# Kernel tuning notes

Measured on AMD Instinct MI355X. Metric: run time of the kernel, lower is better.

Reference implementation:

```python
import jax, jax.numpy as jnp
import numpy as np

DIM = 256
NUM_HEADS = 4
HEAD_DIM = DIM // NUM_HEADS  # 64
SCALE = HEAD_DIM ** -0.5


def _dwconv(x, w, b):
    # x: [B,H,W,C], w: [3,3,1,C] depthwise, stride 2, padding 1
    c = x.shape[-1]
    y = jax.lax.conv_general_dilated(
        x, w, window_strides=(2, 2), padding=((1, 1), (1, 1)),
        dimension_numbers=('NHWC', 'HWIO', 'NHWC'), feature_group_count=c)
    return y + b


def setup_inputs() -> dict:
    key = jax.random.key(0)
    ks = jax.random.split(key, 12)
    s = 0.02
    return {
        'x': jax.random.normal(ks[0], (8, 64, 64, DIM), jnp.float32),
        'q_w': jax.random.normal(ks[1], (DIM, DIM), jnp.float32) * s,
        'q_b': jnp.zeros((DIM,), jnp.float32),
        'k_w': jax.random.normal(ks[2], (DIM, HEAD_DIM), jnp.float32) * s,
        'k_b': jnp.zeros((HEAD_DIM,), jnp.float32),
        'v_w': jax.random.normal(ks[3], (DIM, HEAD_DIM), jnp.float32) * s,
        'v_b': jnp.zeros((HEAD_DIM,), jnp.float32),
        'kconv_w': jax.random.normal(ks[4], (3, 3, 1, HEAD_DIM), jnp.float32) * s,
        'kconv_b': jnp.zeros((HEAD_DIM,), jnp.float32),
        'vconv_w': jax.random.normal(ks[5], (3, 3, 1, HEAD_DIM), jnp.float32) * s,
        'vconv_b': jnp.zeros((HEAD_DIM,), jnp.float32),
        'out_w': jax.random.normal(ks[6], (DIM, DIM), jnp.float32) * s,
        'out_b': jnp.zeros((DIM,), jnp.float32),
    }


def reference(x, q_w, q_b, k_w, k_b, v_w, v_b,
              kconv_w, kconv_b, vconv_w, vconv_b, out_w, out_b):
    B, H, W, _ = x.shape
    S = H * W
    q = x @ q_w + q_b                      # [B,H,W,DIM]
    k = x @ k_w + k_b                      # [B,H,W,HEAD_DIM]
    v = x @ v_w + v_b
    k = _dwconv(k, kconv_w, kconv_b)       # [B,H/2,W/2,HEAD_DIM]
    v = _dwconv(v, vconv_w, vconv_b)
    Kv = (H // 2) * (W // 2)
    q = q.reshape(B, S, NUM_HEADS, HEAD_DIM)
    k = k.reshape(B, Kv, HEAD_DIM)
    v = v.reshape(B, Kv, HEAD_DIM)
    # MQA: single shared K/V head
    attn = jnp.einsum('bqhd,bkd->bhqk', q, k) * SCALE
    attn = jax.nn.softmax(attn, axis=-1)
    out = jnp.einsum('bhqk,bkd->bqhd', attn, v)   # [B,S,nh,hd]
    out = out.reshape(B, S, DIM) @ out_w + out_b
    return out.reshape(B, H, W, DIM)
```

## Files before the change

### kernel.cpp

```cpp
#include <hip/hip_runtime.h>
#include <hip/hip_bf16.h>

typedef __bf16 v8bf __attribute__((ext_vector_type(8)));
typedef float f32x4 __attribute__((ext_vector_type(4)));
typedef float f32x16 __attribute__((ext_vector_type(16)));
typedef int v2i __attribute__((ext_vector_type(2)));
typedef int v4i __attribute__((ext_vector_type(4)));

#define MFMA16(a, b, c) __builtin_amdgcn_mfma_f32_16x16x32_bf16(a, b, c, 0, 0, 0)
#define MFMA32(a, b, c) __builtin_amdgcn_mfma_f32_32x32x16_bf16(a, b, c, 0, 0, 0)
#define GLOAD16(gp, lp)                                                        \
  __builtin_amdgcn_global_load_lds(                                            \
      (const __attribute__((address_space(1))) void*)(gp),                     \
      (__attribute__((address_space(3))) void*)(lp), 16, 0, 0)

#define QSCALE 0.18033688011112042f

__global__ __launch_bounds__(256) void k_cvt_w(const float* __restrict__ qw,
                                               const float* __restrict__ kw,
                                               const float* __restrict__ vw,
                                               const float* __restrict__ ow,
                                               __bf16* __restrict__ wfrag,
                                               __bf16* __restrict__ owfrag) {
  int t = blockIdx.x * 256 + threadIdx.x;
  if (t < 98304) {
    int e = t & 7, idx = t >> 3;
    int l = idx & 63; idx >>= 6;
    int n = idx & 3; idx >>= 2;
    int kk = idx & 7, nb = idx >> 3;
    int nn = nb * 64 + n * 16 + (l & 15);
    int k = kk * 32 + 8 * (l >> 4) + e;
    float v;
    if (nn < 256) v = qw[k * 256 + nn] * QSCALE;
    else if (nn < 320) v = kw[k * 64 + (nn - 256)];
    else v = vw[k * 64 + (nn - 320)];
    wfrag[t] = (__bf16)v;
  } else {
    int u = t - 98304;
    int e = u & 7, idx = u >> 3;
    int l = idx & 63; idx >>= 6;
    int n = idx & 3; idx >>= 2;
    int kk = idx & 7, nb = idx >> 3;
    int nn = nb * 64 + n * 16 + (l & 15);
    int k = kk * 32 + 8 * (l >> 4) + e;
    owfrag[u] = (__bf16)ow[k * 256 + nn];
  }
}

__global__ __launch_bounds__(256) void k_qkv(const float* __restrict__ x,
                                             const __bf16* __restrict__ wfrag,
                                             const float* __restrict__ qb,
                                             const float* __restrict__ kb,
                                             const float* __restrict__ vb,
                                             __bf16* __restrict__ qo,
                                             __bf16* __restrict__ klin,
                                             __bf16* __restrict__ vlin) {
  int bx = blockIdx.x;
  int mb = (bx & 7) * 128 + (bx >> 3);
  int wave = threadIdx.x >> 6, lane = threadIdx.x & 63;
  int rg = wave >> 1, nh = wave & 1;
  int g = lane >> 4, c = lane & 15;
  int r0 = mb * 32 + rg * 16;
  const v8bf* wf = (const v8bf*)wfrag;

  v8bf a[8];
#pragma unroll
  for (int kk = 0; kk < 8; ++kk) {
    const float* ap = x + (size_t)(r0 + c) * 256 + kk * 32 + 8 * g;
    float4 f0 = *(const float4*)ap;
    float4 f1 = *(const float4*)(ap + 4);
    v8bf t;
    t[0] = (__bf16)f0.x; t[1] = (__bf16)f0.y; t[2] = (__bf16)f0.z; t[3] = (__bf16)f0.w;
    t[4] = (__bf16)f1.x; t[5] = (__bf16)f1.y; t[6] = (__bf16)f1.z; t[7] = (__bf16)f1.w;
    a[kk] = t;
  }
#pragma unroll
  for (int ni = 0; ni < 3; ++ni) {
    int nb = nh * 3 + ni;
    int n0 = nb * 64;
    f32x4 acc[4];
#pragma unroll
    for (int n = 0; n < 4; ++n) acc[n] = f32x4{0.f, 0.f, 0.f, 0.f};
#pragma unroll
    for (int kk = 0; kk < 8; ++kk) {
      v8bf bf[4];
#pragma unroll
      for (int n = 0; n < 4; ++n)
        bf[n] = wf[(((nb * 8 + kk) * 4 + n) << 6) | lane];
#pragma unroll
      for (int n = 0; n < 4; ++n) acc[n] = MFMA16(a[kk], bf[n], acc[n]);
    }
#pragma unroll
    for (int n = 0; n < 4; ++n) {
      int col = n0 + n * 16 + c;
      float bias;
      if (col < 256) bias = qb[col] * QSCALE;
      else if (col < 320) bias = kb[col - 256];
      else bias = vb[col - 320];
#pragma unroll
      for (int j = 0; j < 4; ++j) {
        int row = r0 + 4 * g + j;
        float v = acc[n][j] + bias;
        if (col < 256) qo[(size_t)row * 256 + col] = (__bf16)v;
        else if (col < 320) klin[(size_t)row * 64 + (col - 256)] = (__bf16)v;
        else vlin[(size_t)row * 64 + (col - 320)] = (__bf16)v;
      }
    }
  }
}

__global__ __launch_bounds__(256) void k_conv(const __bf16* __restrict__ klin,
                                              const __bf16* __restrict__ vlin,
                                              const float* __restrict__ kw,
                                              const float* __restrict__ kbias,
                                              const float* __restrict__ vw,
                                              const float* __restrict__ vbias,
                                              __bf16* __restrict__ kcS,
                                              __bf16* __restrict__ vcS) {
  int bx = blockIdx.x;
  int phase = bx >> 8;
  int b = (bx >> 5) & 7, tile = bx & 31;
  int u = threadIdx.x;

  if (phase == 0) {
    const __bf16* kin = klin + (size_t)b * 262144;
    int kj = u >> 5, kr = (u & 31) ^ kj;
    float acc[8];
#pragma unroll
    for (int e = 0; e < 8; ++e) acc[e] = kbias[kj * 8 + e];
#pragma unroll
    for (int dy = 0; dy < 3; ++dy) {
      int iy = 2 * tile - 1 + dy;
      if (iy < 0 || iy > 63) continue;
#pragma unroll
      for (int dx = 0; dx < 3; ++dx) {
        int ix = 2 * kr - 1 + dx;
        if (ix < 0 || ix > 63) continue;
        v8bf kv8 = *(const v8bf*)(kin + ((size_t)iy * 64 + ix) * 64 + kj * 8);
        const float* wp = kw + (dy * 3 + dx) * 64 + kj * 8;
#pragma unroll
        for (int e = 0; e < 8; ++e) acc[e] += (float)kv8[e] * wp[e];
      }
    }
    __bf16 o[8];
#pragma unroll
    for (int e = 0; e < 8; ++e) o[e] = (__bf16)acc[e];
    *(v4i*)(kcS + ((size_t)b * 32 + tile) * 2048 + u * 8) = *(v4i*)o;
  } else {
    const __bf16* vin = vlin + (size_t)b * 262144;
    int dt = u >> 7, ks = (u >> 6) & 1, vh = (u >> 5) & 1;
    int cc = (u & 31) ^ (ks * 2 + vh);
    int ch = dt * 32 + cc;
    float vwv[9];
#pragma unroll
    for (int i = 0; i < 9; ++i) vwv[i] = vw[i * 64 + ch];
    float vb0 = vbias[ch];
    __bf16 o[8];
#pragma unroll
    for (int e = 0; e < 8; ++e) {
      int ox = ks * 16 + vh * 8 + e;
      float av = vb0;
#pragma unroll
      for (int dy = 0; dy < 3; ++dy) {
        int iy = 2 * tile - 1 + dy;
        if (iy < 0 || iy > 63) continue;
#pragma unroll
        for (int dx = 0; dx < 3; ++dx) {
          int ix = 2 * ox - 1 + dx;
          if (ix < 0 || ix > 63) continue;
          av += (float)vin[((size_t)iy * 64 + ix) * 64 + ch] * vwv[dy * 3 + dx];
        }
      }
      o[e] = (__bf16)av;
    }
    *(v4i*)(vcS + ((size_t)b * 32 + tile) * 2048 + u * 8) = *(v4i*)o;
  }
}

__global__ __launch_bounds__(256) void k_attn(const __bf16* __restrict__ q,
                                              const __bf16* __restrict__ kcS,
                                              const __bf16* __restrict__ vcS,
                                              const __bf16* __restrict__ owfrag,
                                              const float* __restrict__ ob,
                                              float* __restrict__ out) {
  __shared__ __bf16 SMEM[12288];
  int bx = blockIdx.x;
  int L = (bx & 7) * 128 + (bx >> 3);
  int b = L >> 7, qt = L & 127;
  int wave = threadIdx.x >> 6, lane = threadIdx.x & 63;
  int c = lane & 31, hi = lane >> 5;
  int t = threadIdx.x;
  size_t rowBase = (size_t)b * 4096 + qt * 32;

  const __bf16* kg = kcS + (size_t)b * 65536 + t * 8;
  const __bf16* vg = vcS + (size_t)b * 65536 + t * 8;
  __bf16* kl = &SMEM[t * 8];
  __bf16* vl = &SMEM[2048 + t * 8];

  int Koff[4], Voff[2][2];
#pragma unroll
  for (int kk = 0; kk < 4; ++kk) {
    int j = kk * 2 + hi;
    Koff[kk] = (j * 32 + (c ^ j)) * 8;
  }
#pragma unroll
  for (int ks = 0; ks < 2; ++ks)
#pragma unroll
    for (int dt = 0; dt < 2; ++dt) {
      int j = ks * 2 + hi;
      Voff[ks][dt] = (256 + dt * 128 + ks * 64 + hi * 32 + (c ^ j)) * 8;
    }

  const __bf16* qbase = q + (rowBase + c) * 256 + wave * 64 + hi * 8;
  v8bf Qf[4];
#pragma unroll
  for (int kk = 0; kk < 4; ++kk) Qf[kk] = *(const v8bf*)(qbase + kk * 16);

  f32x16 O0 = {}, O1 = {};
  const f32x16 Z16 = {};
  float ls0 = 0.f, ls1 = 0.f, ls2 = 0.f, ls3 = 0.f;

  GLOAD16(kg, kl);
  GLOAD16(vg, vl);
  GLOAD16(kg + 2048, kl + 4096);
  GLOAD16(vg + 2048, vl + 4096);

  int cur = 0;
  int nxt2 = 2;
  for (int it = 0; it < 32; ++it) {
    if (it < 31) {
      asm volatile("s_waitcnt vmcnt(2)" ::: "memory");
    } else {
      asm volatile("s_waitcnt vmcnt(0)" ::: "memory");
    }
    __builtin_amdgcn_sched_barrier(0);
    __builtin_amdgcn_s_barrier();
    __builtin_amdgcn_sched_barrier(0);
    if (it < 30) {
      GLOAD16(kg + (it + 2) * 2048, kl + nxt2 * 4096);
      GLOAD16(vg + (it + 2) * 2048, vl + nxt2 * 4096);
    }

    const __bf16* base = &SMEM[cur * 4096];
    v8bf Kf[4], Vf[2][2];
#pragma unroll
    for (int kk = 0; kk < 4; ++kk) Kf[kk] = *(const v8bf*)(base + Koff[kk]);
#pragma unroll
    for (int ks = 0; ks < 2; ++ks)
#pragma unroll
      for (int dt = 0; dt < 2; ++dt)
        Vf[ks][dt] = *(const v8bf*)(base + Voff[ks][dt]);

    f32x16 S = MFMA32(Kf[0], Qf[0], Z16);
    S = MFMA32(Kf[1], Qf[1], S);
    S = MFMA32(Kf[2], Qf[2], S);
    S = MFMA32(Kf[3], Qf[3], S);

#pragma unroll
    for (int r = 0; r < 16; ++r) S[r] = __builtin_amdgcn_exp2f(S[r]);
    ls0 += (S[0] + S[1]) + (S[2] + S[3]);
    ls1 += (S[4] + S[5]) + (S[6] + S[7]);
    ls2 += (S[8] + S[9]) + (S[10] + S[11]);
    ls3 += (S[12] + S[13]) + (S[14] + S[15]);

    int w[8];
#pragma unroll
    for (int q2 = 0; q2 < 8; ++q2) {
      int r;
      asm("v_cvt_pk_bf16_f32 %0, %1, %2"
          : "=v"(r) : "v"(S[2 * q2]), "v"(S[2 * q2 + 1]));
      w[q2] = r;
    }
    v2i s1 = __builtin_amdgcn_permlane32_swap(w[2], w[0], false, false);
    v2i s2 = __builtin_amdgcn_permlane32_swap(w[3], w[1], false, false);
    v2i s3 = __builtin_amdgcn_permlane32_swap(w[6], w[4], false, false);
    v2i s4 = __builtin_amdgcn_permlane32_swap(w[7], w[5], false, false);
    v4i pa0i, pa1i;
    pa0i[0] = s1[1]; pa0i[1] = s2[1]; pa0i[2] = s1[0]; pa0i[3] = s2[0];
    pa1i[0] = s3[1]; pa1i[1] = s4[1]; pa1i[2] = s3[0]; pa1i[3] = s4[0];
    v8bf pa0 = *(v8bf*)&pa0i, pa1 = *(v8bf*)&pa1i;

    O0 = MFMA32(pa0, Vf[0][0], O0);
    O1 = MFMA32(pa0, Vf[0][1], O1);
    O0 = MFMA32(pa1, Vf[1][0], O0);
    O1 = MFMA32(pa1, Vf[1][1], O1);

    cur = (cur == 2) ? 0 : cur + 1;
    nxt2 = (nxt2 == 2) ? 0 : nxt2 + 1;
  }

  float lsum = (ls0 + ls1) + (ls2 + ls3);
  float tot = lsum + __shfl_xor(lsum, 32);
  float linv = 1.0f / tot;

  __syncthreads();

  __bf16(*Ot)[264] = (__bf16(*)[264])SMEM;
#pragma unroll
  for (int r = 0; r < 16; ++r) {
    int qr = (r & 3) + 8 * (r >> 2) + 4 * hi;
    float li = __shfl(linv, qr);
    Ot[qr][wave * 64 + c] = (__bf16)(O0[r] * li);
    Ot[qr][wave * 64 + 32 + c] = (__bf16)(O1[r] * li);
  }
  __syncthreads();

  int g = lane >> 4, c16 = lane & 15;
  const v8bf* wf = (const v8bf*)owfrag;
  f32x4 acc[2][4];
#pragma unroll
  for (int m = 0; m < 2; ++m)
#pragma unroll
    for (int n = 0; n < 4; ++n) acc[m][n] = f32x4{0.f, 0.f, 0.f, 0.f};
#pragma unroll
  for (int kk = 0; kk < 8; ++kk) {
    v8bf a0 = *(const v8bf*)&Ot[c16][kk * 32 + 8 * g];
    v8bf a1 = *(const v8bf*)&Ot[16 + c16][kk * 32 + 8 * g];
    v8bf bf[4];
#pragma unroll
    for (int n = 0; n < 4; ++n)
      bf[n] = wf[(((wave * 8 + kk) * 4 + n) << 6) | lane];
#pragma unroll
    for (int n = 0; n < 4; ++n) {
      acc[0][n] = MFMA16(a0, bf[n], acc[0][n]);
      acc[1][n] = MFMA16(a1, bf[n], acc[1][n]);
    }
  }
#pragma unroll
  for (int n = 0; n < 4; ++n) {
    int col = wave * 64 + n * 16 + c16;
    float bias = ob[col];
#pragma unroll
    for (int m = 0; m < 2; ++m)
#pragma unroll
      for (int j = 0; j < 4; ++j) {
        int row = m * 16 + 4 * g + j;
        out[(rowBase + row) * 256 + col] = acc[m][n][j] + bias;
      }
  }
}

extern "C" void kernel_launch(void* const* d_in, const int* in_sizes, int n_in,
                              void* d_out, int out_size, void* d_ws, size_t ws_size,
                              hipStream_t stream) {
  const float* x   = (const float*)d_in[0];
  const float* qw  = (const float*)d_in[1];
  const float* qb  = (const float*)d_in[2];
  const float* kw  = (const float*)d_in[3];
  const float* kb  = (const float*)d_in[4];
  const float* vw  = (const float*)d_in[5];
  const float* vb  = (const float*)d_in[6];
  const float* kcw = (const float*)d_in[7];
  const float* kcb = (const float*)d_in[8];
  const float* vcw = (const float*)d_in[9];
  const float* vcb = (const float*)d_in[10];
  const float* ow  = (const float*)d_in[11];
  const float* ob  = (const float*)d_in[12];
  float* out = (float*)d_out;
  char* ws = (char*)d_ws;

  __bf16* kcS    = (__bf16*)(ws + 0);
  __bf16* vcS    = (__bf16*)(ws + 1048576);
  __bf16* qbuf   = (__bf16*)(ws + 16777216);
  __bf16* klin   = (__bf16*)(ws + 33554432);
  __bf16* vlin   = (__bf16*)(ws + 37748736);
  __bf16* wfrag  = (__bf16*)(ws + 44040192);
  __bf16* owfrag = (__bf16*)(ws + 44236800);

  k_cvt_w<<<640, 256, 0, stream>>>(qw, kw, vw, ow, wfrag, owfrag);
  k_qkv<<<1024, 256, 0, stream>>>(x, wfrag, qb, kb, vb, qbuf, klin, vlin);
  k_conv<<<512, 256, 0, stream>>>(klin, vlin, kcw, kcb, vcw, vcb, kcS, vcS);
  k_attn<<<1024, 256, 0, stream>>>(qbuf, kcS, vcS, owfrag, ob, out);
}
```

Baseline: 89.85 us.

## Double attention block to 64 query rows sharing each K/V tile load

Each attention block now uses 512 threads covering 64 query rows: two row groups of four head-waves. The K/V tiles staged into shared memory are reused by twice as many waves, which halves global K/V traffic per query and halves the block count. Each thread now issues a single async load per stage instead of two, and the out-projection buffer grows to hold 64 rows. The launch bound of 512 threads with 4 blocks per CU may constrain registers, and the larger blocks mean fewer blocks in total across the grid.

```diff
diff --git a/kernel.cpp b/kernel.cpp
--- a/kernel.cpp
+++ b/kernel.cpp
@@ -177,25 +177,26 @@
   }
 }
 
-__global__ __launch_bounds__(256) void k_attn(const __bf16* __restrict__ q,
-                                              const __bf16* __restrict__ kcS,
-                                              const __bf16* __restrict__ vcS,
-                                              const __bf16* __restrict__ owfrag,
-                                              const float* __restrict__ ob,
-                                              float* __restrict__ out) {
-  __shared__ __bf16 SMEM[12288];
+__global__ __launch_bounds__(512, 4) void k_attn(const __bf16* __restrict__ q,
+                                                 const __bf16* __restrict__ kcS,
+                                                 const __bf16* __restrict__ vcS,
+                                                 const __bf16* __restrict__ owfrag,
+                                                 const float* __restrict__ ob,
+                                                 float* __restrict__ out) {
+  __shared__ __bf16 SMEM[16896];
   int bx = blockIdx.x;
-  int L = (bx & 7) * 128 + (bx >> 3);
-  int b = L >> 7, qt = L & 127;
-  int wave = threadIdx.x >> 6, lane = threadIdx.x & 63;
+  int L = (bx & 7) * 64 + (bx >> 3);
+  int b = L >> 6, qt = L & 63;
+  int tid = threadIdx.x;
+  int wave = tid >> 6, lane = tid & 63;
+  int h = wave & 3, rg = wave >> 2;
   int c = lane & 31, hi = lane >> 5;
-  int t = threadIdx.x;
-  size_t rowBase = (size_t)b * 4096 + qt * 32;
-
-  const __bf16* kg = kcS + (size_t)b * 65536 + t * 8;
-  const __bf16* vg = vcS + (size_t)b * 65536 + t * 8;
-  __bf16* kl = &SMEM[t * 8];
-  __bf16* vl = &SMEM[2048 + t * 8];
+  size_t rowBase = (size_t)b * 4096 + qt * 64;
+
+  const __bf16* gsrc = (tid < 256)
+                           ? kcS + (size_t)b * 65536 + tid * 8
+                           : vcS + (size_t)b * 65536 + (tid - 256) * 8;
+  __bf16* ldst = (tid < 256) ? &SMEM[tid * 8] : &SMEM[2048 + (tid - 256) * 8];
 
   int Koff[4], Voff[2][2];
 #pragma unroll
@@ -211,7 +212,7 @@
       Voff[ks][dt] = (256 + dt * 128 + ks * 64 + hi * 32 + (c ^ j)) * 8;
     }
 
-  const __bf16* qbase = q + (rowBase + c) * 256 + wave * 64 + hi * 8;
+  const __bf16* qbase = q + (rowBase + rg * 32 + c) * 256 + h * 64 + hi * 8;
   v8bf Qf[4];
 #pragma unroll
   for (int kk = 0; kk < 4; ++kk) Qf[kk] = *(const v8bf*)(qbase + kk * 16);
@@ -220,16 +221,14 @@
   const f32x16 Z16 = {};
   float ls0 = 0.f, ls1 = 0.f, ls2 = 0.f, ls3 = 0.f;
 
-  GLOAD16(kg, kl);
-  GLOAD16(vg, vl);
-  GLOAD16(kg + 2048, kl + 4096);
-  GLOAD16(vg + 2048, vl + 4096);
+  GLOAD16(gsrc, ldst);
+  GLOAD16(gsrc + 2048, ldst + 4096);
 
   int cur = 0;
   int nxt2 = 2;
   for (int it = 0; it < 32; ++it) {
     if (it < 31) {
-      asm volatile("s_waitcnt vmcnt(2)" ::: "memory");
+      asm volatile("s_waitcnt vmcnt(1)" ::: "memory");
     } else {
       asm volatile("s_waitcnt vmcnt(0)" ::: "memory");
     }
@@ -237,8 +236,7 @@
     __builtin_amdgcn_s_barrier();
     __builtin_amdgcn_sched_barrier(0);
     if (it < 30) {
-      GLOAD16(kg + (it + 2) * 2048, kl + nxt2 * 4096);
-      GLOAD16(vg + (it + 2) * 2048, vl + nxt2 * 4096);
+      GLOAD16(gsrc + (it + 2) * 2048, ldst + nxt2 * 4096);
     }
 
     const __bf16* base = &SMEM[cur * 4096];
@@ -300,8 +298,8 @@
   for (int r = 0; r < 16; ++r) {
     int qr = (r & 3) + 8 * (r >> 2) + 4 * hi;
     float li = __shfl(linv, qr);
-    Ot[qr][wave * 64 + c] = (__bf16)(O0[r] * li);
-    Ot[qr][wave * 64 + 32 + c] = (__bf16)(O1[r] * li);
+    Ot[rg * 32 + qr][h * 64 + c] = (__bf16)(O0[r] * li);
+    Ot[rg * 32 + qr][h * 64 + 32 + c] = (__bf16)(O1[r] * li);
   }
   __syncthreads();
 
@@ -314,12 +312,12 @@
     for (int n = 0; n < 4; ++n) acc[m][n] = f32x4{0.f, 0.f, 0.f, 0.f};
 #pragma unroll
   for (int kk = 0; kk < 8; ++kk) {
-    v8bf a0 = *(const v8bf*)&Ot[c16][kk * 32 + 8 * g];
-    v8bf a1 = *(const v8bf*)&Ot[16 + c16][kk * 32 + 8 * g];
+    v8bf a0 = *(const v8bf*)&Ot[rg * 32 + c16][kk * 32 + 8 * g];
+    v8bf a1 = *(const v8bf*)&Ot[rg * 32 + 16 + c16][kk * 32 + 8 * g];
     v8bf bf[4];
 #pragma unroll
     for (int n = 0; n < 4; ++n)
-      bf[n] = wf[(((wave * 8 + kk) * 4 + n) << 6) | lane];
+      bf[n] = wf[(((h * 8 + kk) * 4 + n) << 6) | lane];
 #pragma unroll
     for (int n = 0; n < 4; ++n) {
       acc[0][n] = MFMA16(a0, bf[n], acc[0][n]);
@@ -328,13 +326,13 @@
   }
 #pragma unroll
   for (int n = 0; n < 4; ++n) {
-    int col = wave * 64 + n * 16 + c16;
+    int col = h * 64 + n * 16 + c16;
     float bias = ob[col];
 #pragma unroll
     for (int m = 0; m < 2; ++m)
 #pragma unroll
       for (int j = 0; j < 4; ++j) {
-        int row = m * 16 + 4 * g + j;
+        int row = rg * 32 + m * 16 + 4 * g + j;
         out[(rowBase + row) * 256 + col] = acc[m][n][j] + bias;
       }
   }
@@ -370,5 +368,5 @@
   k_cvt_w<<<640, 256, 0, stream>>>(qw, kw, vw, ow, wfrag, owfrag);
   k_qkv<<<1024, 256, 0, stream>>>(x, wfrag, qb, kb, vb, qbuf, klin, vlin);
   k_conv<<<512, 256, 0, stream>>>(klin, vlin, kcw, kcb, vcw, vcb, kcS, vcS);
-  k_attn<<<1024, 256, 0, stream>>>(qbuf, kcS, vcS, owfrag, ob, out);
-}
+  k_attn<<<512, 512, 0, stream>>>(qbuf, kcS, vcS, owfrag, ob, out);
+}
```

After: 86.32 us, median of 3. 3.9% less time.

## Load K/V fragments directly from global into registers, drop LDS staging

Applied to the files above, without the earlier changes.

Replaces the triple-buffered global_load_lds staging of K/V tiles and per-iteration barriers with direct per-lane vector loads from global memory (pre-swizzled layout), using a register double-buffer for K and loading V at the start of each iteration. This removes LDS traffic and block-wide synchronisation in the attention loop, shrinks shared memory, and requests 4 blocks per CU via launch bounds. The trade-off is that each wave fetches K/V independently from L2/L1 with less latency hiding for V, and register pressure rises under the tighter occupancy bound.

```diff
diff --git a/kernel.cpp b/kernel.cpp
--- a/kernel.cpp
+++ b/kernel.cpp
@@ -9,10 +9,6 @@
 
 #define MFMA16(a, b, c) __builtin_amdgcn_mfma_f32_16x16x32_bf16(a, b, c, 0, 0, 0)
 #define MFMA32(a, b, c) __builtin_amdgcn_mfma_f32_32x32x16_bf16(a, b, c, 0, 0, 0)
-#define GLOAD16(gp, lp)                                                        \
-  __builtin_amdgcn_global_load_lds(                                            \
-      (const __attribute__((address_space(1))) void*)(gp),                     \
-      (__attribute__((address_space(3))) void*)(lp), 16, 0, 0)
 
 #define QSCALE 0.18033688011112042f
 
@@ -177,27 +173,21 @@
   }
 }
 
-__global__ __launch_bounds__(256) void k_attn(const __bf16* __restrict__ q,
-                                              const __bf16* __restrict__ kcS,
-                                              const __bf16* __restrict__ vcS,
-                                              const __bf16* __restrict__ owfrag,
-                                              const float* __restrict__ ob,
-                                              float* __restrict__ out) {
-  __shared__ __bf16 SMEM[12288];
+__global__ __launch_bounds__(256, 4) void k_attn(const __bf16* __restrict__ q,
+                                                 const __bf16* __restrict__ kcS,
+                                                 const __bf16* __restrict__ vcS,
+                                                 const __bf16* __restrict__ owfrag,
+                                                 const float* __restrict__ ob,
+                                                 float* __restrict__ out) {
+  __shared__ __bf16 SMEM[8448];
   int bx = blockIdx.x;
   int L = (bx & 7) * 128 + (bx >> 3);
   int b = L >> 7, qt = L & 127;
   int wave = threadIdx.x >> 6, lane = threadIdx.x & 63;
   int c = lane & 31, hi = lane >> 5;
-  int t = threadIdx.x;
   size_t rowBase = (size_t)b * 4096 + qt * 32;
 
-  const __bf16* kg = kcS + (size_t)b * 65536 + t * 8;
-  const __bf16* vg = vcS + (size_t)b * 65536 + t * 8;
-  __bf16* kl = &SMEM[t * 8];
-  __bf16* vl = &SMEM[2048 + t * 8];
-
-  int Koff[4], Voff[2][2];
+  int Koff[4], Voffg[2][2];
 #pragma unroll
   for (int kk = 0; kk < 4; ++kk) {
     int j = kk * 2 + hi;
@@ -208,8 +198,10 @@
 #pragma unroll
     for (int dt = 0; dt < 2; ++dt) {
       int j = ks * 2 + hi;
-      Voff[ks][dt] = (256 + dt * 128 + ks * 64 + hi * 32 + (c ^ j)) * 8;
-    }
+      Voffg[ks][dt] = (dt * 128 + ks * 64 + hi * 32 + (c ^ j)) * 8;
+    }
+  const __bf16* kbase = kcS + (size_t)b * 65536;
+  const __bf16* vbase = vcS + (size_t)b * 65536;
 
   const __bf16* qbase = q + (rowBase + c) * 256 + wave * 64 + hi * 8;
   v8bf Qf[4];
@@ -220,80 +212,60 @@
   const f32x16 Z16 = {};
   float ls0 = 0.f, ls1 = 0.f, ls2 = 0.f, ls3 = 0.f;
 
-  GLOAD16(kg, kl);
-  GLOAD16(vg, vl);
-  GLOAD16(kg + 2048, kl + 4096);
-  GLOAD16(vg + 2048, vl + 4096);
-
-  int cur = 0;
-  int nxt2 = 2;
-  for (int it = 0; it < 32; ++it) {
-    if (it < 31) {
-      asm volatile("s_waitcnt vmcnt(2)" ::: "memory");
-    } else {
-      asm volatile("s_waitcnt vmcnt(0)" ::: "memory");
-    }
-    __builtin_amdgcn_sched_barrier(0);
-    __builtin_amdgcn_s_barrier();
-    __builtin_amdgcn_sched_barrier(0);
-    if (it < 30) {
-      GLOAD16(kg + (it + 2) * 2048, kl + nxt2 * 4096);
-      GLOAD16(vg + (it + 2) * 2048, vl + nxt2 * 4096);
-    }
-
-    const __bf16* base = &SMEM[cur * 4096];
-    v8bf Kf[4], Vf[2][2];
-#pragma unroll
-    for (int kk = 0; kk < 4; ++kk) Kf[kk] = *(const v8bf*)(base + Koff[kk]);
-#pragma unroll
-    for (int ks = 0; ks < 2; ++ks)
-#pragma unroll
-      for (int dt = 0; dt < 2; ++dt)
-        Vf[ks][dt] = *(const v8bf*)(base + Voff[ks][dt]);
-
-    f32x16 S = MFMA32(Kf[0], Qf[0], Z16);
-    S = MFMA32(Kf[1], Qf[1], S);
-    S = MFMA32(Kf[2], Qf[2], S);
-    S = MFMA32(Kf[3], Qf[3], S);
-
-#pragma unroll
-    for (int r = 0; r < 16; ++r) S[r] = __builtin_amdgcn_exp2f(S[r]);
-    ls0 += (S[0] + S[1]) + (S[2] + S[3]);
-    ls1 += (S[4] + S[5]) + (S[6] + S[7]);
-    ls2 += (S[8] + S[9]) + (S[10] + S[11]);
-    ls3 += (S[12] + S[13]) + (S[14] + S[15]);
-
-    int w[8];
-#pragma unroll
-    for (int q2 = 0; q2 < 8; ++q2) {
-      int r;
-      asm("v_cvt_pk_bf16_f32 %0, %1, %2"
-          : "=v"(r) : "v"(S[2 * q2]), "v"(S[2 * q2 + 1]));
-      w[q2] = r;
-    }
-    v2i s1 = __builtin_amdgcn_permlane32_swap(w[2], w[0], false, false);
-    v2i s2 = __builtin_amdgcn_permlane32_swap(w[3], w[1], false, false);
-    v2i s3 = __builtin_amdgcn_permlane32_swap(w[6], w[4], false, false);
-    v2i s4 = __builtin_amdgcn_permlane32_swap(w[7], w[5], false, false);
-    v4i pa0i, pa1i;
-    pa0i[0] = s1[1]; pa0i[1] = s2[1]; pa0i[2] = s1[0]; pa0i[3] = s2[0];
-    pa1i[0] = s3[1]; pa1i[1] = s4[1]; pa1i[2] = s3[0]; pa1i[3] = s4[0];
-    v8bf pa0 = *(v8bf*)&pa0i, pa1 = *(v8bf*)&pa1i;
-
-    O0 = MFMA32(pa0, Vf[0][0], O0);
-    O1 = MFMA32(pa0, Vf[0][1], O1);
-    O0 = MFMA32(pa1, Vf[1][0], O0);
-    O1 = MFMA32(pa1, Vf[1][1], O1);
-
-    cur = (cur == 2) ? 0 : cur + 1;
-    nxt2 = (nxt2 == 2) ? 0 : nxt2 + 1;
-  }
+#define ATTN_ITER(IT, KCUR, KNXT, PF)                                          \
+  do {                                                                         \
+    v8bf Vf[2][2];                                                             \
+    _Pragma("unroll") for (int ks = 0; ks < 2; ++ks)                           \
+        _Pragma("unroll") for (int dt = 0; dt < 2; ++dt) Vf[ks][dt] =          \
+        *(const v8bf*)(vbase + (IT) * 2048 + Voffg[ks][dt]);                   \
+    if (PF) {                                                                  \
+      _Pragma("unroll") for (int kk = 0; kk < 4; ++kk) KNXT[kk] =              \
+          *(const v8bf*)(kbase + ((IT) + 1) * 2048 + Koff[kk]);                \
+    }                                                                          \
+    f32x16 S = MFMA32(KCUR[0], Qf[0], Z16);                                    \
+    S = MFMA32(KCUR[1], Qf[1], S);                                             \
+    S = MFMA32(KCUR[2], Qf[2], S);                                             \
+    S = MFMA32(KCUR[3], Qf[3], S);                                             \
+    _Pragma("unroll") for (int r = 0; r < 16; ++r) S[r] =                      \
+        __builtin_amdgcn_exp2f(S[r]);                                          \
+    ls0 += (S[0] + S[1]) + (S[2] + S[3]);                                      \
+    ls1 += (S[4] + S[5]) + (S[6] + S[7]);                                      \
+    ls2 += (S[8] + S[9]) + (S[10] + S[11]);                                    \
+    ls3 += (S[12] + S[13]) + (S[14] + S[15]);                                  \
+    int w[8];                                                                  \
+    _Pragma("unroll") for (int q2 = 0; q2 < 8; ++q2) {                         \
+      int r;                                                                   \
+      asm("v_cvt_pk_bf16_f32 %0, %1, %2"                                       \
+          : "=v"(r) : "v"(S[2 * q2]), "v"(S[2 * q2 + 1]));                     \
+      w[q2] = r;                                                               \
+    }                                                                          \
+    v2i s1 = __builtin_amdgcn_permlane32_swap(w[2], w[0], false, false);       \
+    v2i s2 = __builtin_amdgcn_permlane32_swap(w[3], w[1], false, false);       \
+    v2i s3 = __builtin_amdgcn_permlane32_swap(w[6], w[4], false, false);       \
+    v2i s4 = __builtin_amdgcn_permlane32_swap(w[7], w[5], false, false);       \
+    v4i pa0i, pa1i;                                                            \
+    pa0i[0] = s1[1]; pa0i[1] = s2[1]; pa0i[2] = s1[0]; pa0i[3] = s2[0];        \
+    pa1i[0] = s3[1]; pa1i[1] = s4[1]; pa1i[2] = s3[0]; pa1i[3] = s4[0];        \
+    v8bf pa0 = *(v8bf*)&pa0i, pa1 = *(v8bf*)&pa1i;                             \
+    O0 = MFMA32(pa0, Vf[0][0], O0);                                            \
+    O1 = MFMA32(pa0, Vf[0][1], O1);                                            \
+    O0 = MFMA32(pa1, Vf[1][0], O0);                                            \
+    O1 = MFMA32(pa1, Vf[1][1], O1);                                            \
+  } while (0)
+
+  v8bf Ka[4], Kb[4];
+#pragma unroll
+  for (int kk = 0; kk < 4; ++kk) Ka[kk] = *(const v8bf*)(kbase + Koff[kk]);
+
+  for (int j = 0; j < 16; ++j) {
+    ATTN_ITER(2 * j, Ka, Kb, true);
+    ATTN_ITER(2 * j + 1, Kb, Ka, (j < 15));
+  }
+#undef ATTN_ITER
 
   float lsum = (ls0 + ls1) + (ls2 + ls3);
   float tot = lsum + __shfl_xor(lsum, 32);
   float linv = 1.0f / tot;
-
-  __syncthreads();
 
   __bf16(*Ot)[264] = (__bf16(*)[264])SMEM;
 #pragma unroll
```

Result: slower. 106.8 us (+18.9%).
